# Kernel optimization log

Hardware: AMD Instinct MI355X
Metric: run time of the kernel (lower is better)

Reference implementation:

```python
import jax, jax.numpy as jnp
import numpy as np

B, S, MD, H = 8, 1024, 1024, 16
D = MD // H  # 64
# Faithful to torch: scale = (dim_per_head // num_heads) ** -0.5 (a quirk, not 1/sqrt(D))
SCALE = float((D // H) ** (-0.5))


def setup_inputs() -> dict:
    k0 = jax.random.key(0)
    ks = jax.random.split(k0, 11)
    w = 1.0 / np.sqrt(MD)
    mk = lambda k, shape, s: jax.random.normal(k, shape, dtype=jnp.float32) * s
    return {
        "query": mk(ks[0], (B, S, MD), 1.0),
        "key": mk(ks[1], (B, S, MD), 1.0),
        "value": mk(ks[2], (B, S, MD), 1.0),
        "Wq": mk(ks[3], (MD, MD), w), "bq": mk(ks[4], (MD,), w),
        "Wk": mk(ks[5], (MD, MD), w), "bk": mk(ks[6], (MD,), w),
        "Wv": mk(ks[7], (MD, MD), w), "bv": mk(ks[8], (MD,), w),
        "Wo": mk(ks[9], (MD, MD), w), "bo": mk(ks[10], (MD,), w),
    }


def reference(query, key, value, Wq, bq, Wk, bk, Wv, bv, Wo, bo):
    # Dropout is identity in eval mode (deterministic reference).
    Bq, T, _ = query.shape
    Sk = key.shape[1]
    q = query @ Wq + bq   # [B, T, H*D]
    k = key @ Wk + bk     # [B, S, H*D]
    v = value @ Wv + bv
    # Faithful replication of torch .view(B*H, -1, D): plain row-major reshape
    # (NOT a head transpose -- it chunks sequence/head indices together).
    q = q.reshape(Bq * H, T, D)
    k = k.reshape(Bq * H, Sk, D)
    v = v.reshape(Bq * H, Sk, D)
    attn = jnp.einsum('btd,bsd->bts', q, k) * SCALE          # [B*H, T, S]
    p = jax.nn.softmax(attn, axis=-1)
    ctx = jnp.einsum('bts,bsd->btd', p, v).reshape(Bq, T, H * D)
    output = ctx @ Wo + bo                                    # [B, T, MD]
    a = attn.reshape(Bq, H, T, Sk)
    attn_post = jax.nn.sigmoid(a).sum(axis=1) / H             # [B, T, S]
    return output, attn_post
```

## Files before the change

kernel.cpp:

```cpp
#include <hip/hip_runtime.h>


typedef __attribute__((ext_vector_type(8))) short bf16x8;
typedef __attribute__((ext_vector_type(4))) float f32x4;

static __device__ __forceinline__ short f2bf(float f) {
  union { float f; unsigned u; } v; v.f = f;
  unsigned lsb = (v.u >> 16) & 1u;
  v.u += 0x7fffu + lsb;
  return (short)(v.u >> 16);
}

static __device__ __forceinline__ float bf2f(short s) {
  union { float f; unsigned u; } v;
  v.u = ((unsigned)(unsigned short)s) << 16;
  return v.f;
}

static __device__ __forceinline__ short f2bf_rhu(float f) {
  union { float f; unsigned u; } v; v.f = f;
  v.u += 0x8000u;
  return (short)(v.u >> 16);
}

static __device__ __forceinline__ float exp2_hw(float x) {
  float r;
  asm("v_exp_f32 %0, %1" : "=v"(r) : "v"(x));
  return r;
}

#define L2E_HALF 0.72134752f

#define GLDS16(gp, lp) __builtin_amdgcn_global_load_lds( \
    (const __attribute__((address_space(1))) void*)(gp), \
    (__attribute__((address_space(3))) void*)(lp), 16, 0, 0)

struct Ptr4 { const float* s[4]; short* d[4]; };
struct Ptr3 { const float* s[3]; short* d[3]; };
struct QkvArgs { const short* A[3]; const short* B[3]; const float* bias[3]; short* C[3]; };

__global__ __launch_bounds__(256) void convt4(Ptr4 a)
{
  const float* __restrict__ src = a.s[blockIdx.z];
  short* __restrict__ dst = a.d[blockIdx.z];
  __shared__ float T[64][65];
  const int tid = threadIdx.x;
  const int c0 = blockIdx.x * 64, r0 = blockIdx.y * 64;
  {
    const int rr = tid >> 4, cc = (tid & 15) * 4;
    for (int i = 0; i < 4; ++i) {
      int row = rr + i * 16;
      const float4 v = *(const float4*)(src + (size_t)(r0 + row) * 1024 + c0 + cc);
      T[row][cc] = v.x; T[row][cc + 1] = v.y; T[row][cc + 2] = v.z; T[row][cc + 3] = v.w;
    }
  }
  __syncthreads();
  {
    const int rr = tid >> 3, cc = (tid & 7) * 8;
    for (int i = 0; i < 2; ++i) {
      int row = rr + i * 32;
      bf16x8 v;
      for (int j = 0; j < 8; ++j) v[j] = f2bf(T[cc + j][row]);
      *(bf16x8*)(dst + (size_t)(c0 + row) * 1024 + r0 + cc) = v;
    }
  }
}

__global__ __launch_bounds__(256) void cvt3(Ptr3 a)
{
  const float* __restrict__ src = a.s[blockIdx.z];
  short* __restrict__ dst = a.d[blockIdx.z];
  const size_t i = ((size_t)blockIdx.x * 256 + threadIdx.x) * 8;
  const float4 v0 = *(const float4*)(src + i);
  const float4 v1 = *(const float4*)(src + i + 4);
  bf16x8 o;
  o[0] = f2bf(v0.x); o[1] = f2bf(v0.y); o[2] = f2bf(v0.z); o[3] = f2bf(v0.w);
  o[4] = f2bf(v1.x); o[5] = f2bf(v1.y); o[6] = f2bf(v1.z); o[7] = f2bf(v1.w);
  *(bf16x8*)(dst + i) = o;
}

__global__ __launch_bounds__(256) void add_post(
    float* __restrict__ ap, const short* __restrict__ part)
{
  const size_t i = ((size_t)blockIdx.x * 256 + threadIdx.x) * 8;
  float4 a0 = *(float4*)(ap + i);
  float4 a1 = *(float4*)(ap + i + 4);
  const bf16x8 p = *(const bf16x8*)(part + i);
  a0.x += bf2f(p[0]); a0.y += bf2f(p[1]); a0.z += bf2f(p[2]); a0.w += bf2f(p[3]);
  a1.x += bf2f(p[4]); a1.y += bf2f(p[5]); a1.z += bf2f(p[6]); a1.w += bf2f(p[7]);
  *(float4*)(ap + i) = a0;
  *(float4*)(ap + i + 4) = a1;
}

__global__ __launch_bounds__(256) void transp_v(
    const short* __restrict__ src, short* __restrict__ dst)
{
  __shared__ short T[64][72];
  const int g = blockIdx.y, t0 = blockIdx.x * 64;
  const short* s = src + (size_t)g * 65536 + (size_t)t0 * 64;
  short* d = dst + (size_t)g * 65536 + t0;
  const int r = threadIdx.x >> 3, c = (threadIdx.x & 7) * 8;
  for (int i = 0; i < 2; ++i) {
    bf16x8 v = *(const bf16x8*)(s + (size_t)(r + i * 32) * 64 + c);
    *(bf16x8*)(&T[r + i * 32][c]) = v;
  }
  __syncthreads();
  for (int i = 0; i < 2; ++i) {
    int dr = r + i * 32;
    bf16x8 v;
    for (int j = 0; j < 8; ++j) v[j] = T[c + j][dr];
    *(bf16x8*)(d + (size_t)dr * 1024 + c) = v;
  }
}

static __device__ __forceinline__ void gemm_body(
    const short* __restrict__ A, const short* __restrict__ BT,
    const float* __restrict__ bias, void* __restrict__ Cp, int mode)
{
  __shared__ short As[2][128 * 64];
  __shared__ short Bs[2][128 * 64];
  const int K = 1024, N = 1024;
  const int tid = threadIdx.x;
  const int lane = tid & 63, wave = tid >> 6;
  const int quad = lane >> 4, l16 = lane & 15;
  const int wm = (wave & 1) * 64, wn = (wave >> 1) * 64;
  const int lin = blockIdx.y * 64 + blockIdx.x;
  const int xcd = lin & 7, idx = lin >> 3;
  const int bx = xcd * 8 + (idx & 7);
  const int by = idx >> 3;
  const int bm = bx * 128, bn = by * 128;

  f32x4 acc[4][4] = {};

  const int s_row = tid >> 3;
  const int s_col = (tid & 7) * 8;
  const int lds_base = wave * 512;

  for (int i = 0; i < 4; ++i) {
    int row = s_row + i * 32;
    GLDS16(A + (size_t)(bm + row) * K + s_col, &As[0][i * 2048 + lds_base]);
    GLDS16(BT + (size_t)(bn + row) * K + s_col, &Bs[0][i * 2048 + lds_base]);
  }
  __syncthreads();

  int cur = 0;
  for (int t = 0; t < 16; ++t) {
    if (t < 15) {
      const int k0 = (t + 1) * 64;
      for (int i = 0; i < 4; ++i) {
        int row = s_row + i * 32;
        GLDS16(A + (size_t)(bm + row) * K + k0 + s_col, &As[cur ^ 1][i * 2048 + lds_base]);
        GLDS16(BT + (size_t)(bn + row) * K + k0 + s_col, &Bs[cur ^ 1][i * 2048 + lds_base]);
      }
    }
    for (int ks = 0; ks < 2; ++ks) {
      bf16x8 af[4], bfr[4];
      for (int mi = 0; mi < 4; ++mi)
        af[mi] = *(const bf16x8*)(&As[cur][(wm + mi * 16 + l16) * 64 + ks * 32 + quad * 8]);
      for (int ni = 0; ni < 4; ++ni)
        bfr[ni] = *(const bf16x8*)(&Bs[cur][(wn + ni * 16 + l16) * 64 + ks * 32 + quad * 8]);
      for (int mi = 0; mi < 4; ++mi)
        for (int ni = 0; ni < 4; ++ni)
          acc[mi][ni] = __builtin_amdgcn_mfma_f32_16x16x32_bf16(af[mi], bfr[ni], acc[mi][ni], 0, 0, 0);
    }
    __syncthreads();
    cur ^= 1;
  }

  for (int ni = 0; ni < 4; ++ni) {
    int col = bn + wn + ni * 16 + l16;
    float bv = bias[col];
    for (int mi = 0; mi < 4; ++mi) {
      int row0 = bm + wm + mi * 16 + quad * 4;
      for (int r = 0; r < 4; ++r) {
        int row = row0 + r;
        float fv = acc[mi][ni][r] + bv;
        if (mode == 2) ((float*)Cp)[(size_t)row * N + col] = fv;
        else           ((short*)Cp)[(size_t)row * N + col] = f2bf(fv);
      }
    }
  }
}

__global__ __launch_bounds__(256) void gemm_bt16(
    const short* __restrict__ A, const short* __restrict__ BT,
    const float* __restrict__ bias, void* __restrict__ Cp, int mode)
{
  gemm_body(A, BT, bias, Cp, mode);
}

__global__ __launch_bounds__(256) void gemm_qkv(QkvArgs a)
{
  const int z = blockIdx.z;
  gemm_body(a.A[z], a.B[z], a.bias[z], a.C[z], 0);
}

__global__ __launch_bounds__(256, 1) void attn_fused12(
    const short* __restrict__ Qp, const short* __restrict__ Kp,
    const short* __restrict__ VpT,
    short* __restrict__ ctx,
    float* __restrict__ attn_post,
    short* __restrict__ part)
{
  __shared__ short Plds[32][1032];
  __shared__ float red[32][4];

  const int tid = threadIdx.x;
  const int wave = tid >> 6, lane = tid & 63;
  const int quad = lane >> 4, l16 = lane & 15;
  const int orig = blockIdx.x;
  const int b = orig & 7;
  const int hg = (orig >> 3) & 1;
  const int t0 = (orig >> 4) * 32;
  const int sbase = wave * 256;

  float sig[2][16][4] = {};

  for (int h = hg * 8; h < hg * 8 + 8; ++h) {
    const int g = b * 16 + h;
    const short* Qg = Qp + (size_t)g * 65536;
    const short* Kg = Kp + (size_t)g * 65536;
    const short* Vg = VpT + (size_t)g * 65536;

    bf16x8 aq[2][2];
#pragma unroll
    for (int tt = 0; tt < 2; ++tt) {
      aq[tt][0] = *(const bf16x8*)(Qg + (t0 + tt * 16 + l16) * 64 + quad * 8);
      aq[tt][1] = *(const bf16x8*)(Qg + (t0 + tt * 16 + l16) * 64 + 32 + quad * 8);
    }

    float rsum[2][4] = {};

    bf16x8 kb0[4], kb1[4];
#pragma unroll
    for (int t = 0; t < 4; ++t) {
      int s = sbase + t * 16;
      kb0[t] = *(const bf16x8*)(Kg + (s + l16) * 64 + quad * 8);
      kb1[t] = *(const bf16x8*)(Kg + (s + l16) * 64 + 32 + quad * 8);
    }
#pragma unroll
    for (int tile = 0; tile < 16; ++tile) {
      const int slot = tile & 3;
      bf16x8 bk0 = kb0[slot], bk1 = kb1[slot];
      if (tile < 12) {
        int s = sbase + (tile + 4) * 16;
        kb0[slot] = *(const bf16x8*)(Kg + (s + l16) * 64 + quad * 8);
        kb1[slot] = *(const bf16x8*)(Kg + (s + l16) * 64 + 32 + quad * 8);
      }
#pragma unroll
      for (int tt = 0; tt < 2; ++tt) {
        f32x4 c = {0.f, 0.f, 0.f, 0.f};
        c = __builtin_amdgcn_mfma_f32_16x16x32_bf16(aq[tt][0], bk0, c, 0, 0, 0);
        c = __builtin_amdgcn_mfma_f32_16x16x32_bf16(aq[tt][1], bk1, c, 0, 0, 0);
#pragma unroll
        for (int r = 0; r < 4; ++r) {
          float e = exp2_hw(c[r] * L2E_HALF);
          rsum[tt][r] += e;
          Plds[tt * 16 + quad * 4 + r][sbase + tile * 16 + l16] = f2bf_rhu(e);
          sig[tt][tile][r] += e * __builtin_amdgcn_rcpf(1.f + e);
        }
      }
    }
#pragma unroll
    for (int tt = 0; tt < 2; ++tt)
      for (int r = 0; r < 4; ++r)
        for (int mask = 1; mask < 16; mask <<= 1)
          rsum[tt][r] += __shfl_xor(rsum[tt][r], mask, 64);
    if (l16 == 0)
#pragma unroll
      for (int tt = 0; tt < 2; ++tt)
        for (int r = 0; r < 4; ++r)
          red[tt * 16 + quad * 4 + r][wave] = rsum[tt][r];
    __syncthreads();

    const short* Vw = Vg + (size_t)(wave * 16 + l16) * 1024;
    f32x4 acc[2][2] = {};
#pragma unroll
    for (int sl = 0; sl < 32; ++sl) {
      bf16x8 v  = *(const bf16x8*)(Vw + sl * 32 + quad * 8);
      bf16x8 p0 = *(const bf16x8*)(&Plds[l16][sl * 32 + quad * 8]);
      bf16x8 p1 = *(const bf16x8*)(&Plds[16 + l16][sl * 32 + quad * 8]);
      acc[0][sl & 1] = __builtin_amdgcn_mfma_f32_16x16x32_bf16(p0, v, acc[0][sl & 1], 0, 0, 0);
      acc[1][sl & 1] = __builtin_amdgcn_mfma_f32_16x16x32_bf16(p1, v, acc[1][sl & 1], 0, 0, 0);
    }

    short* ctxg = ctx + (size_t)g * 65536 + t0 * 64;
#pragma unroll
    for (int tt = 0; tt < 2; ++tt)
      for (int r = 0; r < 4; ++r) {
        int row = tt * 16 + quad * 4 + r;
        float s4 = red[row][0] + red[row][1] + red[row][2] + red[row][3];
        float inv = __builtin_amdgcn_rcpf(s4);
        float cval = (acc[tt][0][r] + acc[tt][1][r]) * inv;
        ctxg[row * 64 + wave * 16 + l16] = f2bf(cval);
      }
    __syncthreads();
  }

  if (hg == 0) {
    float* ap_out = attn_post + (size_t)b * 1048576 + (size_t)t0 * 1024;
#pragma unroll
    for (int tt = 0; tt < 2; ++tt)
      for (int tile = 0; tile < 16; ++tile)
        for (int r = 0; r < 4; ++r)
          ap_out[(tt * 16 + quad * 4 + r) * 1024 + sbase + tile * 16 + l16] =
              sig[tt][tile][r] * 0.0625f;
  } else {
    short* pp = part + (size_t)b * 1048576 + (size_t)t0 * 1024;
#pragma unroll
    for (int tt = 0; tt < 2; ++tt)
      for (int tile = 0; tile < 16; ++tile)
        for (int r = 0; r < 4; ++r)
          pp[(tt * 16 + quad * 4 + r) * 1024 + sbase + tile * 16 + l16] =
              f2bf(sig[tt][tile][r] * 0.0625f);
  }
}

extern "C" void kernel_launch(void* const* d_in, const int* in_sizes, int n_in,
                              void* d_out, int out_size, void* d_ws, size_t ws_size,
                              hipStream_t stream) {
  const float* query = (const float*)d_in[0];
  const float* key   = (const float*)d_in[1];
  const float* value = (const float*)d_in[2];
  const float* Wq = (const float*)d_in[3]; const float* bq = (const float*)d_in[4];
  const float* Wk = (const float*)d_in[5]; const float* bk = (const float*)d_in[6];
  const float* Wv = (const float*)d_in[7]; const float* bv = (const float*)d_in[8];
  const float* Wo = (const float*)d_in[9]; const float* bo = (const float*)d_in[10];

  float* out0 = (float*)d_out;
  float* attn_post = out0 + (8u << 20);

  short* WqT = (short*)d_ws;
  short* WkT = WqT + (1u << 20);
  short* WvT = WkT + (1u << 20);
  short* WoT = WvT + (1u << 20);
  short* Qp  = WoT + (1u << 20);
  short* Kp  = Qp + (8u << 20);
  short* VpT = Kp + (8u << 20);

  dim3 blk(256);
  dim3 ggrid(64, 8);
  const size_t NEED_BIG = (size_t)(60u << 20) * 2;

  convt4<<<dim3(16, 16, 4), blk, 0, stream>>>(
      Ptr4{{Wq, Wk, Wv, Wo}, {WqT, WkT, WvT, WoT}});

  short* ctx;
  short* part;
  if (ws_size >= NEED_BIG) {
    short* Xq = VpT + (8u << 20);
    short* Xk = Xq + (8u << 20);
    short* Xv = Xk + (8u << 20);
    short* Vflat = Xv + (8u << 20);
    ctx = Xq;
    part = Vflat;

    cvt3<<<dim3(4096, 1, 3), blk, 0, stream>>>(Ptr3{{query, key, value}, {Xq, Xk, Xv}});
    gemm_qkv<<<dim3(64, 8, 3), blk, 0, stream>>>(
        QkvArgs{{Xq, Xk, Xv}, {WqT, WkT, WvT}, {bq, bk, bv}, {Qp, Kp, Vflat}});
    transp_v<<<dim3(16, 128), blk, 0, stream>>>(Vflat, VpT);
  } else {
    short* Xin = VpT + (8u << 20);
    short* Vflat = Xin + (8u << 20);
    ctx = Xin;
    part = Vflat;

    cvt3<<<dim3(4096, 1, 1), blk, 0, stream>>>(Ptr3{{query, query, query}, {Xin, Xin, Xin}});
    gemm_bt16<<<ggrid, blk, 0, stream>>>(Xin, WqT, bq, Qp, 0);
    cvt3<<<dim3(4096, 1, 1), blk, 0, stream>>>(Ptr3{{key, key, key}, {Xin, Xin, Xin}});
    gemm_bt16<<<ggrid, blk, 0, stream>>>(Xin, WkT, bk, Kp, 0);
    cvt3<<<dim3(4096, 1, 1), blk, 0, stream>>>(Ptr3{{value, value, value}, {Xin, Xin, Xin}});
    gemm_bt16<<<ggrid, blk, 0, stream>>>(Xin, WvT, bv, Vflat, 0);
    transp_v<<<dim3(16, 128), blk, 0, stream>>>(Vflat, VpT);
  }

  attn_fused12<<<dim3(512), blk, 0, stream>>>(Qp, Kp, VpT, ctx, attn_post, part);
  add_post<<<dim3(4096), blk, 0, stream>>>(attn_post, part);
  gemm_bt16<<<ggrid, blk, 0, stream>>>(ctx, WoT, bo, out0, 2);
}
```

Measured before the change: 469.8 us.

## Chunk attention key axis into four 256-wide slices to shrink LDS P buffer

The fused attention kernel now processes the 1024 keys in four 256-column chunks. Each wave computes its 64-column slice of P for a chunk, then all waves run the P·V MFMAs on that chunk before moving on. This cuts the LDS P buffer from about 66KB to about 17KB and spreads the V loads across the head loop. The cost is two barriers per chunk, eight per head instead of two, and the row-sum buffer is double-buffered by head parity to drop the trailing barrier.

```diff
diff --git a/kernel.cpp b/kernel.cpp
--- a/kernel.cpp
+++ b/kernel.cpp
@@ -195,15 +195,15 @@
   gemm_body(a.A[z], a.B[z], a.bias[z], a.C[z], 0);
 }
 
-__global__ __launch_bounds__(256, 1) void attn_fused12(
+__global__ __launch_bounds__(256, 1) void attn_fused13(
     const short* __restrict__ Qp, const short* __restrict__ Kp,
     const short* __restrict__ VpT,
     short* __restrict__ ctx,
     float* __restrict__ attn_post,
     short* __restrict__ part)
 {
-  __shared__ short Plds[32][1032];
-  __shared__ float red[32][4];
+  __shared__ short Plds[32][264];
+  __shared__ float red[2][32][4];
 
   const int tid = threadIdx.x;
   const int wave = tid >> 6, lane = tid & 63;
@@ -212,7 +212,7 @@
   const int b = orig & 7;
   const int hg = (orig >> 3) & 1;
   const int t0 = (orig >> 4) * 32;
-  const int sbase = wave * 256;
+  const int wbase = wave * 64;
 
   float sig[2][16][4] = {};
 
@@ -221,6 +221,7 @@
     const short* Qg = Qp + (size_t)g * 65536;
     const short* Kg = Kp + (size_t)g * 65536;
     const short* Vg = VpT + (size_t)g * 65536;
+    const short* Vw = Vg + (size_t)(wave * 16 + l16) * 1024;
 
     bf16x8 aq[2][2];
 #pragma unroll
@@ -230,37 +231,48 @@
     }
 
     float rsum[2][4] = {};
-
-    bf16x8 kb0[4], kb1[4];
-#pragma unroll
-    for (int t = 0; t < 4; ++t) {
-      int s = sbase + t * 16;
-      kb0[t] = *(const bf16x8*)(Kg + (s + l16) * 64 + quad * 8);
-      kb1[t] = *(const bf16x8*)(Kg + (s + l16) * 64 + 32 + quad * 8);
-    }
-#pragma unroll
-    for (int tile = 0; tile < 16; ++tile) {
-      const int slot = tile & 3;
-      bf16x8 bk0 = kb0[slot], bk1 = kb1[slot];
-      if (tile < 12) {
-        int s = sbase + (tile + 4) * 16;
-        kb0[slot] = *(const bf16x8*)(Kg + (s + l16) * 64 + quad * 8);
-        kb1[slot] = *(const bf16x8*)(Kg + (s + l16) * 64 + 32 + quad * 8);
-      }
-#pragma unroll
-      for (int tt = 0; tt < 2; ++tt) {
-        f32x4 c = {0.f, 0.f, 0.f, 0.f};
-        c = __builtin_amdgcn_mfma_f32_16x16x32_bf16(aq[tt][0], bk0, c, 0, 0, 0);
-        c = __builtin_amdgcn_mfma_f32_16x16x32_bf16(aq[tt][1], bk1, c, 0, 0, 0);
-#pragma unroll
-        for (int r = 0; r < 4; ++r) {
-          float e = exp2_hw(c[r] * L2E_HALF);
-          rsum[tt][r] += e;
-          Plds[tt * 16 + quad * 4 + r][sbase + tile * 16 + l16] = f2bf_rhu(e);
-          sig[tt][tile][r] += e * __builtin_amdgcn_rcpf(1.f + e);
+    f32x4 acc[2][2] = {};
+
+#pragma unroll
+    for (int c = 0; c < 4; ++c) {
+      const int sb = c * 256 + wbase;
+
+      bf16x8 kb0[4], kb1[4];
+#pragma unroll
+      for (int t = 0; t < 4; ++t) {
+        int s = sb + t * 16;
+        kb0[t] = *(const bf16x8*)(Kg + (s + l16) * 64 + quad * 8);
+        kb1[t] = *(const bf16x8*)(Kg + (s + l16) * 64 + 32 + quad * 8);
+      }
+#pragma unroll
+      for (int tile = 0; tile < 4; ++tile) {
+#pragma unroll
+        for (int tt = 0; tt < 2; ++tt) {
+          f32x4 cc = {0.f, 0.f, 0.f, 0.f};
+          cc = __builtin_amdgcn_mfma_f32_16x16x32_bf16(aq[tt][0], kb0[tile], cc, 0, 0, 0);
+          cc = __builtin_amdgcn_mfma_f32_16x16x32_bf16(aq[tt][1], kb1[tile], cc, 0, 0, 0);
+#pragma unroll
+          for (int r = 0; r < 4; ++r) {
+            float e = exp2_hw(cc[r] * L2E_HALF);
+            rsum[tt][r] += e;
+            Plds[tt * 16 + quad * 4 + r][wbase + tile * 16 + l16] = f2bf_rhu(e);
+            sig[tt][c * 4 + tile][r] += e * __builtin_amdgcn_rcpf(1.f + e);
+          }
         }
       }
-    }
+      __syncthreads();
+
+#pragma unroll
+      for (int sl = 0; sl < 8; ++sl) {
+        bf16x8 v  = *(const bf16x8*)(Vw + c * 256 + sl * 32 + quad * 8);
+        bf16x8 p0 = *(const bf16x8*)(&Plds[l16][sl * 32 + quad * 8]);
+        bf16x8 p1 = *(const bf16x8*)(&Plds[16 + l16][sl * 32 + quad * 8]);
+        acc[0][sl & 1] = __builtin_amdgcn_mfma_f32_16x16x32_bf16(p0, v, acc[0][sl & 1], 0, 0, 0);
+        acc[1][sl & 1] = __builtin_amdgcn_mfma_f32_16x16x32_bf16(p1, v, acc[1][sl & 1], 0, 0, 0);
+      }
+      __syncthreads();
+    }
+
 #pragma unroll
     for (int tt = 0; tt < 2; ++tt)
       for (int r = 0; r < 4; ++r)
@@ -270,49 +282,42 @@
 #pragma unroll
       for (int tt = 0; tt < 2; ++tt)
         for (int r = 0; r < 4; ++r)
-          red[tt * 16 + quad * 4 + r][wave] = rsum[tt][r];
+          red[h & 1][tt * 16 + quad * 4 + r][wave] = rsum[tt][r];
     __syncthreads();
-
-    const short* Vw = Vg + (size_t)(wave * 16 + l16) * 1024;
-    f32x4 acc[2][2] = {};
-#pragma unroll
-    for (int sl = 0; sl < 32; ++sl) {
-      bf16x8 v  = *(const bf16x8*)(Vw + sl * 32 + quad * 8);
-      bf16x8 p0 = *(const bf16x8*)(&Plds[l16][sl * 32 + quad * 8]);
-      bf16x8 p1 = *(const bf16x8*)(&Plds[16 + l16][sl * 32 + quad * 8]);
-      acc[0][sl & 1] = __builtin_amdgcn_mfma_f32_16x16x32_bf16(p0, v, acc[0][sl & 1], 0, 0, 0);
-      acc[1][sl & 1] = __builtin_amdgcn_mfma_f32_16x16x32_bf16(p1, v, acc[1][sl & 1], 0, 0, 0);
-    }
 
     short* ctxg = ctx + (size_t)g * 65536 + t0 * 64;
 #pragma unroll
     for (int tt = 0; tt < 2; ++tt)
       for (int r = 0; r < 4; ++r) {
         int row = tt * 16 + quad * 4 + r;
-        float s4 = red[row][0] + red[row][1] + red[row][2] + red[row][3];
+        float s4 = red[h & 1][row][0] + red[h & 1][row][1]
+                 + red[h & 1][row][2] + red[h & 1][row][3];
         float inv = __builtin_amdgcn_rcpf(s4);
         float cval = (acc[tt][0][r] + acc[tt][1][r]) * inv;
         ctxg[row * 64 + wave * 16 + l16] = f2bf(cval);
       }
-    __syncthreads();
   }
 
   if (hg == 0) {
     float* ap_out = attn_post + (size_t)b * 1048576 + (size_t)t0 * 1024;
 #pragma unroll
     for (int tt = 0; tt < 2; ++tt)
-      for (int tile = 0; tile < 16; ++tile)
+      for (int k = 0; k < 16; ++k) {
+        int ci = k >> 2, tile = k & 3;
         for (int r = 0; r < 4; ++r)
-          ap_out[(tt * 16 + quad * 4 + r) * 1024 + sbase + tile * 16 + l16] =
-              sig[tt][tile][r] * 0.0625f;
+          ap_out[(tt * 16 + quad * 4 + r) * 1024 + ci * 256 + wbase + tile * 16 + l16] =
+              sig[tt][k][r] * 0.0625f;
+      }
   } else {
     short* pp = part + (size_t)b * 1048576 + (size_t)t0 * 1024;
 #pragma unroll
     for (int tt = 0; tt < 2; ++tt)
-      for (int tile = 0; tile < 16; ++tile)
+      for (int k = 0; k < 16; ++k) {
+        int ci = k >> 2, tile = k & 3;
         for (int r = 0; r < 4; ++r)
-          pp[(tt * 16 + quad * 4 + r) * 1024 + sbase + tile * 16 + l16] =
-              f2bf(sig[tt][tile][r] * 0.0625f);
+          pp[(tt * 16 + quad * 4 + r) * 1024 + ci * 256 + wbase + tile * 16 + l16] =
+              f2bf(sig[tt][k][r] * 0.0625f);
+      }
   }
 }
 
@@ -374,7 +379,7 @@
     transp_v<<<dim3(16, 128), blk, 0, stream>>>(Vflat, VpT);
   }
 
-  attn_fused12<<<dim3(512), blk, 0, stream>>>(Qp, Kp, VpT, ctx, attn_post, part);
+  attn_fused13<<<dim3(512), blk, 0, stream>>>(Qp, Kp, VpT, ctx, attn_post, part);
   add_post<<<dim3(4096), blk, 0, stream>>>(attn_post, part);
   gemm_bt16<<<ggrid, blk, 0, stream>>>(ctx, WoT, bo, out0, 2);
 }
```

Measured after the change: 560.9 us. +19.4%, slower.
